# Kernel tuning notes

Hardware: AMD Instinct MI355X
Metric: run time of the kernel (lower is better)

The kernel has to match this reference:

```python
import jax, jax.numpy as jnp
import numpy as np

N, T, DIN, E, D, L, G = 50000, 1, 7, 800000, 64, 3, 64


def _lin(key, fi, fo):
    k1, k2 = jax.random.split(key)
    s = 1.0 / np.sqrt(fi)
    return (jax.random.uniform(k1, (fi, fo), jnp.float32, -s, s),
            jax.random.uniform(k2, (fo,), jnp.float32, -s, s))


def setup_inputs() -> dict:
    key = jax.random.key(0)
    ks = jax.random.split(key, 16)
    x = jax.random.normal(ks[0], (N, T, DIN), jnp.float32)
    edge_index = jax.random.randint(ks[1], (2, E), 0, N).astype(jnp.int64)
    edge_attr = jax.random.uniform(ks[2], (E, T), jnp.float32)
    batch = jnp.sort(jax.random.randint(ks[3], (N,), 0, G)).astype(jnp.int64)
    degree = jax.random.uniform(ks[4], (N,), jnp.float32)
    W_en, b_en = _lin(ks[5], DIN, D)
    W_ene, b_ene = _lin(ks[6], DIN + 1, D - 1)
    W_agg, b_agg = _lin(ks[7], D, D)
    Wm = []; bm = []; Wu = []; bu = []
    for l in range(L):
        w, b = _lin(jax.random.fold_in(ks[8], l), 2 * D, D); Wm.append(w); bm.append(b)
        w, b = _lin(jax.random.fold_in(ks[9], l), 2 * D, D); Wu.append(w); bu.append(b)
    Wm = jnp.stack(Wm); bm = jnp.stack(bm); Wu = jnp.stack(Wu); bu = jnp.stack(bu)
    W_g, b_g = _lin(ks[10], D, D)
    W_r, b_r = _lin(ks[11], 2 * D, 1)
    return dict(x=x, edge_index=edge_index, edge_attr=edge_attr, batch=batch,
                degree=degree, num_graphs=G,
                W_en=W_en, b_en=b_en, W_ene=W_ene, b_ene=b_ene,
                W_agg=W_agg, b_agg=b_agg, Wm=Wm, bm=bm, Wu=Wu, bu=bu,
                W_g=W_g, b_g=b_g, W_r=W_r, b_r=b_r)


def _scatter_mean(vals, idx, n):
    # vals: [M, T, F] -> [n, T, F]; empty segments -> 0 (count clamped to 1)
    s = jax.ops.segment_sum(vals, idx, num_segments=n)
    c = jax.ops.segment_sum(jnp.ones((vals.shape[0], 1, 1), vals.dtype), idx, num_segments=n)
    return s / jnp.maximum(c, 1.0)


def reference(x, edge_index, edge_attr, batch, degree, num_graphs,
              W_en, b_en, W_ene, b_ene, W_agg, b_agg,
              Wm, bm, Wu, bu, W_g, b_g, W_r, b_r):
    relu = jax.nn.relu
    col, row = edge_index[0], edge_index[1]
    n = x.shape[0]
    x_emb = relu(x @ W_en + b_en)                                   # [N,T,D]
    # node+edge embedding: gather source nodes, append edge_attr, mean over dst
    ne_in = jnp.concatenate([x[col], edge_attr[:, :, None]], axis=-1)  # [E,T,DIN+1]
    node_edge = _scatter_mean(ne_in, row, n)                        # [N,T,DIN+1]
    node_edge = relu(node_edge @ W_ene + b_ene)                     # [N,T,D-1]
    deg_max = jax.ops.segment_max(degree, batch, num_segments=num_graphs)
    degree_norm = deg_max[batch][:, None, None]                     # [N,1,1] -> broadcast over T
    degree_norm = jnp.broadcast_to(degree_norm, (n, node_edge.shape[1], 1))
    x_agg_emb = relu(jnp.concatenate([node_edge, degree_norm], axis=-1) @ W_agg + b_agg)
    for l in range(Wm.shape[0]):
        x_agg = _scatter_mean(edge_attr[:, :, None] * x_emb[col], row, n)   # [N,T,D]
        m = relu(jnp.concatenate([x_agg, x_agg_emb], axis=-1) @ Wm[l] + bm[l])
        x_emb = relu(jnp.concatenate([x_emb, m], axis=-1) @ Wu[l] + bu[l])
    g_agg = _scatter_mean(x_emb, batch, num_graphs)                 # [G,T,D]
    g_agg = g_agg @ W_g + b_g
    inp = jnp.concatenate([g_agg[batch], x_emb], axis=-1)           # [N,T,2D]
    q = relu(inp) @ W_r + b_r                                       # [N,T,1]
    return jnp.squeeze(q, axis=-1)                                  # [N,T]
```

## Files before the change

kernel.cpp:

```cpp
#include <hip/hip_runtime.h>

constexpr int NN  = 50000;
constexpr int EE  = 800000;
constexpr int GG  = 64;
constexpr int LL  = 3;

__device__ __forceinline__ float reluf(float x) { return x > 0.f ? x : 0.f; }

__global__ void k_count(const int* __restrict__ ei, int* __restrict__ cnt,
                        int* __restrict__ rel) {
    int e = blockIdx.x * blockDim.x + threadIdx.x;
    if (e >= EE) return;
    rel[e] = atomicAdd(&cnt[ei[EE + e]], 1);
}

__global__ void k_scan1(const int* __restrict__ cnt, int* __restrict__ off,
                        int* __restrict__ bsum,
                        const int* __restrict__ batch, const float* __restrict__ degree,
                        unsigned* __restrict__ degmax_u) {
    __shared__ int s[256];
    __shared__ unsigned smax[GG];
    int t = threadIdx.x, blk = blockIdx.x;
    if (t < GG) smax[t] = 0u;
    int base = blk * 1024 + t * 4;
    int v[4], tot = 0;
#pragma unroll
    for (int j = 0; j < 4; j++) {
        int i = base + j;
        v[j] = (i < NN) ? cnt[i] : 0;
        tot += v[j];
    }
    s[t] = tot;
    __syncthreads();
    {
        int curb = -1; unsigned cur = 0u;
#pragma unroll
        for (int j = 0; j < 4; j++) {
            int i = base + j;
            if (i < NN) {
                int b = batch[i];
                unsigned d = __float_as_uint(degree[i]);
                if (b != curb) {
                    if (curb >= 0) atomicMax(&smax[curb], cur);
                    curb = b; cur = d;
                } else if (d > cur) cur = d;
            }
        }
        if (curb >= 0) atomicMax(&smax[curb], cur);
    }
    for (int d = 1; d < 256; d <<= 1) {
        int a = (t >= d) ? s[t - d] : 0;
        __syncthreads();
        s[t] += a;
        __syncthreads();
    }
    int run = s[t] - tot;
#pragma unroll
    for (int j = 0; j < 4; j++) {
        int i = base + j;
        if (i <= NN) off[i] = run;
        run += v[j];
    }
    if (t == 255) bsum[blk] = s[255];
    __syncthreads();
    if (t < GG && smax[t] != 0u) atomicMax(&degmax_u[t], smax[t]);
}
__global__ void k_scan2(int* __restrict__ bsum, int nb) {
    if (threadIdx.x == 0) {
        int run = 0;
        for (int b = 0; b < nb; b++) { int t = bsum[b]; bsum[b] = run; run += t; }
    }
}
__global__ void k_scan3(int* __restrict__ off, const int* __restrict__ bsum) {
    int i = blockIdx.x * blockDim.x + threadIdx.x;
    if (i <= NN) off[i] += bsum[i >> 10];
}

__global__ void k_fill(const int* __restrict__ ei, const float* __restrict__ ea,
                       const int* __restrict__ off, const int* __restrict__ rel,
                       int2* __restrict__ sorted) {
    int e = blockIdx.x * blockDim.x + threadIdx.x;
    if (e >= EE) return;
    int col = ei[e];
    int row = ei[EE + e];
    sorted[off[row] + rel[e]] = make_int2(col, __float_as_int(ea[e]));
}

__global__ void k_nesum(const float* __restrict__ x, const int2* __restrict__ sorted,
                        const int* __restrict__ off, float* __restrict__ ne_sum) {
    int gwave = (blockIdx.x * blockDim.x + threadIdx.x) >> 6;
    int lane = threadIdx.x & 63;
    int sub = lane >> 3;
    int f = lane & 7;
    int node = gwave * 8 + sub;
    if (node >= NN) return;
    int jb = off[node], je = off[node + 1];
    float a0 = 0.f, a1 = 0.f, a2 = 0.f, a3 = 0.f;
    int j = jb;
    for (; j + 4 <= je; j += 4) {
        int2 p0 = sorted[j], p1 = sorted[j + 1], p2 = sorted[j + 2], p3 = sorted[j + 3];
        a0 += (f < 7) ? x[(size_t)p0.x * 7 + f] : __int_as_float(p0.y);
        a1 += (f < 7) ? x[(size_t)p1.x * 7 + f] : __int_as_float(p1.y);
        a2 += (f < 7) ? x[(size_t)p2.x * 7 + f] : __int_as_float(p2.y);
        a3 += (f < 7) ? x[(size_t)p3.x * 7 + f] : __int_as_float(p3.y);
    }
    for (; j < je; j++) {
        int2 p = sorted[j];
        a0 += (f < 7) ? x[(size_t)p.x * 7 + f] : __int_as_float(p.y);
    }
    ne_sum[(size_t)node * 8 + f] = (a0 + a1) + (a2 + a3);
}

__global__ __launch_bounds__(256) void k_node_pre(
        const float* __restrict__ x, const int* __restrict__ cnt,
        const float* __restrict__ ne_sum, const unsigned* __restrict__ degmax_u,
        const int* __restrict__ batch,
        const float* __restrict__ W_en, const float* __restrict__ b_en,
        const float* __restrict__ W_ene, const float* __restrict__ b_ene,
        float* __restrict__ x_emb, float* __restrict__ agg_in) {
    __shared__ float sWen[7 * 64], sben[64];
    __shared__ float sWene[8 * 63], sbene[63];
    for (int i = threadIdx.x; i < 7 * 64; i += 256) sWen[i] = W_en[i];
    for (int i = threadIdx.x; i < 64; i += 256) sben[i] = b_en[i];
    for (int i = threadIdx.x; i < 8 * 63; i += 256) sWene[i] = W_ene[i];
    for (int i = threadIdx.x; i < 63; i += 256) sbene[i] = b_ene[i];
    __syncthreads();
    int lane = threadIdx.x & 63;
    int slot = threadIdx.x >> 6;
    int wave = blockIdx.x * 4 + slot;
    int nw = gridDim.x * 4;
    for (int i = wave; i < NN; i += nw) {
        float acc = sben[lane];
#pragma unroll
        for (int k = 0; k < 7; k++) acc += x[(size_t)i * 7 + k] * sWen[k * 64 + lane];
        x_emb[(size_t)i * 64 + lane] = reluf(acc);
        float c = (float)cnt[i]; if (c < 1.f) c = 1.f;
        float rc = 1.f / c;
        int oo = lane < 63 ? lane : 0;
        float na = sbene[oo];
#pragma unroll
        for (int k = 0; k < 8; k++) na += (ne_sum[(size_t)i * 8 + k] * rc) * sWene[k * 63 + oo];
        na = reluf(na);
        float dn = __uint_as_float(degmax_u[batch[i]]);
        agg_in[(size_t)i * 64 + lane] = (lane < 63) ? na : dn;
    }
}

template <int MODE>
__global__ __launch_bounds__(256) void k_mv64(
        const float* __restrict__ in, const float* __restrict__ W,
        const float* __restrict__ b, const float* __restrict__ tmp,
        float* __restrict__ out, int nwaves) {
    __shared__ float sbuf[4][2][64];
    int slot = threadIdx.x >> 6;
    int gwave = (blockIdx.x * blockDim.x + threadIdx.x) >> 6;
    int lane = threadIdx.x & 63;
    int per = (NN + nwaves - 1) / nwaves;
    int n0 = gwave * per;
    int n1 = n0 + per; if (n1 > NN) n1 = NN;
    if (n0 >= n1) return;
    float w[64];
#pragma unroll
    for (int k = 0; k < 64; k++) w[k] = W[(size_t)k * 64 + lane];
    float bias = (MODE == 0) ? 0.f : b[lane];
    sbuf[slot][0][lane] = in[(size_t)n0 * 64 + lane];
    int cntn = n1 - n0;
    for (int i = 0; i < cntn; i++) {
        int n = n0 + i;
        size_t oA = (size_t)n * 64 + lane;
        float tv = (MODE == 1) ? tmp[oA] : 0.f;
        float vnext = 0.f;
        if (i + 1 < cntn) vnext = in[(size_t)(n + 1) * 64 + lane];
        const float* bufp = &sbuf[slot][i & 1][0];
        float a0 = 0.f, a1 = 0.f;
#pragma unroll
        for (int kb = 0; kb < 64; kb += 8) {
            float4 x0 = *(const float4*)(bufp + kb);
            float4 x1 = *(const float4*)(bufp + kb + 4);
            a0 = fmaf(x0.x, w[kb + 0], a0); a1 = fmaf(x0.y, w[kb + 1], a1);
            a0 = fmaf(x0.z, w[kb + 2], a0); a1 = fmaf(x0.w, w[kb + 3], a1);
            a0 = fmaf(x1.x, w[kb + 4], a0); a1 = fmaf(x1.y, w[kb + 5], a1);
            a0 = fmaf(x1.z, w[kb + 6], a0); a1 = fmaf(x1.w, w[kb + 7], a1);
        }
        float r = a0 + a1;
        if (MODE == 0)      out[oA] = r;
        else if (MODE == 1) out[oA] = reluf(r + tv + bias);
        else                out[oA] = reluf(r + bias);
        if (i + 1 < cntn) sbuf[slot][(i + 1) & 1][lane] = vnext;
    }
}

__global__ __launch_bounds__(256) void k_layer_agg(
        const float* __restrict__ xemb, const int* __restrict__ off,
        const int* __restrict__ cnt, const int2* __restrict__ sorted,
        float* __restrict__ xagg) {
    int lane = threadIdx.x & 63;
    int slot = threadIdx.x >> 6;
    int wave = blockIdx.x * 4 + slot;
    int nw = gridDim.x * 4;
    for (int i = wave; i < NN; i += nw) {
        int jb = off[i], je = off[i + 1];
        float a0 = 0.f, a1 = 0.f, a2 = 0.f, a3 = 0.f;
        float a4 = 0.f, a5 = 0.f, a6 = 0.f, a7 = 0.f;
        int j = jb;
        for (; j + 8 <= je; j += 8) {
            int2 p0 = sorted[j + 0], p1 = sorted[j + 1];
            int2 p2 = sorted[j + 2], p3 = sorted[j + 3];
            int2 p4 = sorted[j + 4], p5 = sorted[j + 5];
            int2 p6 = sorted[j + 6], p7 = sorted[j + 7];
            a0 = fmaf(__int_as_float(p0.y), xemb[(size_t)p0.x * 64 + lane], a0);
            a1 = fmaf(__int_as_float(p1.y), xemb[(size_t)p1.x * 64 + lane], a1);
            a2 = fmaf(__int_as_float(p2.y), xemb[(size_t)p2.x * 64 + lane], a2);
            a3 = fmaf(__int_as_float(p3.y), xemb[(size_t)p3.x * 64 + lane], a3);
            a4 = fmaf(__int_as_float(p4.y), xemb[(size_t)p4.x * 64 + lane], a4);
            a5 = fmaf(__int_as_float(p5.y), xemb[(size_t)p5.x * 64 + lane], a5);
            a6 = fmaf(__int_as_float(p6.y), xemb[(size_t)p6.x * 64 + lane], a6);
            a7 = fmaf(__int_as_float(p7.y), xemb[(size_t)p7.x * 64 + lane], a7);
        }
        if (j < je) {
            int jl = je - 1;
            int2 p0 = sorted[j + 0];
            int2 p1 = sorted[min(j + 1, jl)];
            int2 p2 = sorted[min(j + 2, jl)];
            int2 p3 = sorted[min(j + 3, jl)];
            int2 p4 = sorted[min(j + 4, jl)];
            int2 p5 = sorted[min(j + 5, jl)];
            int2 p6 = sorted[min(j + 6, jl)];
            int2 p7 = sorted[min(j + 7, jl)];
            float s0 = __int_as_float(p0.y);
            float s1 = (j + 1 < je) ? __int_as_float(p1.y) : 0.f;
            float s2 = (j + 2 < je) ? __int_as_float(p2.y) : 0.f;
            float s3 = (j + 3 < je) ? __int_as_float(p3.y) : 0.f;
            float s4 = (j + 4 < je) ? __int_as_float(p4.y) : 0.f;
            float s5 = (j + 5 < je) ? __int_as_float(p5.y) : 0.f;
            float s6 = (j + 6 < je) ? __int_as_float(p6.y) : 0.f;
            float s7 = (j + 7 < je) ? __int_as_float(p7.y) : 0.f;
            a0 = fmaf(s0, xemb[(size_t)p0.x * 64 + lane], a0);
            a1 = fmaf(s1, xemb[(size_t)p1.x * 64 + lane], a1);
            a2 = fmaf(s2, xemb[(size_t)p2.x * 64 + lane], a2);
            a3 = fmaf(s3, xemb[(size_t)p3.x * 64 + lane], a3);
            a4 = fmaf(s4, xemb[(size_t)p4.x * 64 + lane], a4);
            a5 = fmaf(s5, xemb[(size_t)p5.x * 64 + lane], a5);
            a6 = fmaf(s6, xemb[(size_t)p6.x * 64 + lane], a6);
            a7 = fmaf(s7, xemb[(size_t)p7.x * 64 + lane], a7);
        }
        float acc = ((a0 + a1) + (a2 + a3)) + ((a4 + a5) + (a6 + a7));
        float c = (float)cnt[i]; if (c < 1.f) c = 1.f;
        xagg[(size_t)i * 64 + lane] = acc * (1.f / c);
    }
}

constexpr int CHUNK = 32;
__global__ void k_graph_sum(const float* __restrict__ xemb, const int* __restrict__ batch,
                            float* __restrict__ g_sum, int* __restrict__ g_cnt) {
    int wave = (blockIdx.x * blockDim.x + threadIdx.x) >> 6;
    int lane = threadIdx.x & 63;
    int i0 = wave * CHUNK;
    if (i0 >= NN) return;
    int i1 = i0 + CHUNK; if (i1 > NN) i1 = NN;
    int curb = batch[i0];
    float acc = 0.f;
    int ncnt = 0;
    for (int i = i0; i < i1; i++) {
        int b = batch[i];
        if (b != curb) {
            unsafeAtomicAdd(&g_sum[curb * 64 + lane], acc);
            if (lane == 0) atomicAdd(&g_cnt[curb], ncnt);
            acc = 0.f; ncnt = 0; curb = b;
        }
        acc += xemb[(size_t)i * 64 + lane];
        ncnt++;
    }
    unsafeAtomicAdd(&g_sum[curb * 64 + lane], acc);
    if (lane == 0) atomicAdd(&g_cnt[curb], ncnt);
}

__global__ void k_graph_emb(const float* __restrict__ g_sum, const int* __restrict__ g_cnt,
                            const float* __restrict__ W_g, const float* __restrict__ b_g,
                            float* __restrict__ g_agg) {
    __shared__ float sin[4 * 64];
    int lane = threadIdx.x & 63;
    int slot = threadIdx.x >> 6;
    int g = blockIdx.x * 4 + slot;
    if (g >= GG) return;
    float c = (float)g_cnt[g]; if (c < 1.f) c = 1.f;
    sin[slot * 64 + lane] = g_sum[g * 64 + lane] * (1.f / c);
    __syncthreads();
    float acc = b_g[lane];
    for (int k = 0; k < 64; k++) acc += sin[slot * 64 + k] * W_g[k * 64 + lane];
    g_agg[g * 64 + lane] = acc;
}

__global__ void k_readout(const float* __restrict__ g_agg, const float* __restrict__ xemb,
                          const int* __restrict__ batch,
                          const float* __restrict__ W_r, const float* __restrict__ b_r,
                          float* __restrict__ out) {
    int i = blockIdx.x * blockDim.x + threadIdx.x;
    if (i >= NN) return;
    int b = batch[i];
    float acc = b_r[0];
    const float* ga = g_agg + (size_t)b * 64;
    const float* xe = xemb + (size_t)i * 64;
#pragma unroll 8
    for (int k = 0; k < 64; k++) acc += reluf(ga[k]) * W_r[k];
#pragma unroll 8
    for (int k = 0; k < 64; k++) acc += reluf(xe[k]) * W_r[64 + k];
    out[i] = acc;
}

extern "C" void kernel_launch(void* const* d_in, const int* in_sizes, int n_in,
                              void* d_out, int out_size, void* d_ws, size_t ws_size,
                              hipStream_t stream) {
    const float* x      = (const float*)d_in[0];
    const int*   ei     = (const int*)d_in[1];
    const float* ea     = (const float*)d_in[2];
    const int*   batch  = (const int*)d_in[3];
    const float* degree = (const float*)d_in[4];
    const float* W_en  = (const float*)d_in[6];
    const float* b_en  = (const float*)d_in[7];
    const float* W_ene = (const float*)d_in[8];
    const float* b_ene = (const float*)d_in[9];
    const float* W_agg = (const float*)d_in[10];
    const float* b_agg = (const float*)d_in[11];
    const float* Wm    = (const float*)d_in[12];
    const float* bm    = (const float*)d_in[13];
    const float* Wu    = (const float*)d_in[14];
    const float* bu    = (const float*)d_in[15];
    const float* W_g   = (const float*)d_in[16];
    const float* b_g   = (const float*)d_in[17];
    const float* W_r   = (const float*)d_in[18];
    const float* b_r   = (const float*)d_in[19];
    float* out = (float*)d_out;

    char* ws = (char*)d_ws;
    size_t o = 0;
    int*      cnt      = (int*)(ws + o * 4);      o += NN;
    unsigned* degmax_u = (unsigned*)(ws + o * 4); o += GG;
    float*    g_sum    = (float*)(ws + o * 4);    o += GG * 64;
    int*      g_cnt    = (int*)(ws + o * 4);      o += GG;
    size_t zero_bytes = o * 4;
    int*      off      = (int*)(ws + o * 4);      o += NN + 1;
    int*      bsum     = (int*)(ws + o * 4);      o += 64;
    int*      rel      = (int*)(ws + o * 4);      o += EE;
    float*    ne_sum   = (float*)(ws + o * 4);    o += (size_t)NN * 8;
    o = (o + 1) & ~(size_t)1;
    int2*     sorted   = (int2*)(ws + o * 4);     o += (size_t)EE * 2;
    float*    agg_in   = (float*)(ws + o * 4);    o += (size_t)NN * 64;
    float*    xae      = (float*)(ws + o * 4);    o += (size_t)NN * 64;
    float*    xA       = (float*)(ws + o * 4);    o += (size_t)NN * 64;
    float*    xB       = (float*)(ws + o * 4);    o += (size_t)NN * 64;
    float*    xagg     = (float*)(ws + o * 4);    o += (size_t)NN * 64;
    float*    mbuf     = (float*)(ws + o * 4);    o += (size_t)NN * 64;
    float*    tmpb     = (float*)(ws + o * 4);    o += (size_t)NN * 64;
    float*    g_agg    = (float*)(ws + o * 4);    o += GG * 64;

    hipMemsetAsync(d_ws, 0, zero_bytes, stream);

    const int NB_SCAN = 49;
    const int MV_BLOCKS = 1024;
    const int MV_WAVES = MV_BLOCKS * 4;
    k_count<<<(EE + 255) / 256, 256, 0, stream>>>(ei, cnt, rel);
    k_scan1<<<NB_SCAN, 256, 0, stream>>>(cnt, off, bsum, batch, degree, degmax_u);
    k_scan2<<<1, 64, 0, stream>>>(bsum, NB_SCAN);
    k_scan3<<<(NN + 256) / 256, 256, 0, stream>>>(off, bsum);
    k_fill<<<(EE + 255) / 256, 256, 0, stream>>>(ei, ea, off, rel, sorted);
    k_nesum<<<((NN + 7) / 8 * 64 + 255) / 256, 256, 0, stream>>>(x, sorted, off, ne_sum);
    k_node_pre<<<512, 256, 0, stream>>>(x, cnt, ne_sum, degmax_u, batch,
                                        W_en, b_en, W_ene, b_ene, xA, agg_in);
    k_mv64<2><<<MV_BLOCKS, 256, 0, stream>>>(agg_in, W_agg, b_agg, nullptr, xae, MV_WAVES);
    const float* cur = xA;
    float* nxt = xB;
    for (int l = 0; l < LL; l++) {
        const float* WmL = Wm + (size_t)l * 128 * 64;
        const float* WuL = Wu + (size_t)l * 128 * 64;
        k_layer_agg<<<2048, 256, 0, stream>>>(cur, off, cnt, sorted, xagg);
        k_mv64<0><<<MV_BLOCKS, 256, 0, stream>>>(xagg, WmL, nullptr, nullptr, tmpb, MV_WAVES);
        k_mv64<1><<<MV_BLOCKS, 256, 0, stream>>>(xae, WmL + 64 * 64, bm + l * 64, tmpb,
                                                 mbuf, MV_WAVES);
        k_mv64<0><<<MV_BLOCKS, 256, 0, stream>>>(cur, WuL, nullptr, nullptr, tmpb, MV_WAVES);
        k_mv64<1><<<MV_BLOCKS, 256, 0, stream>>>(mbuf, WuL + 64 * 64, bu + l * 64, tmpb,
                                                 nxt, MV_WAVES);
        float* t = (float*)cur; cur = nxt; nxt = t;
    }
    int gs_waves = (NN + CHUNK - 1) / CHUNK;
    k_graph_sum<<<(gs_waves * 64 + 255) / 256, 256, 0, stream>>>(cur, batch, g_sum, g_cnt);
    k_graph_emb<<<16, 256, 0, stream>>>(g_sum, g_cnt, W_g, b_g, g_agg);
    k_readout<<<(NN + 255) / 256, 256, 0, stream>>>(g_agg, cur, batch, W_r, b_r, out);
}
```

Baseline: 489.3 us.

## Fuse split 64-wide matvecs into 128-wide kernels and fold graph sum into last layer

Replaces the pairs of 64-input matvec kernels (which passed partial sums through a temp buffer) with a single 128-input kernel that reads both concatenated halves, removing the tmp buffer round trip and halving launches per layer. The W_agg matvec is folded into k_node_pre using wave shuffles, the graph node count moves into the scan kernel, and the graph sum is accumulated inside the final update kernel, removing k_graph_sum. The 128-register weight array raises register pressure, with launch bounds and block count adjusted to compensate.

After: 483.2 us. About the same (-1.2%).

```diff
diff --git a/kernel.cpp b/kernel.cpp
--- a/kernel.cpp
+++ b/kernel.cpp
@@ -17,11 +17,12 @@
 __global__ void k_scan1(const int* __restrict__ cnt, int* __restrict__ off,
                         int* __restrict__ bsum,
                         const int* __restrict__ batch, const float* __restrict__ degree,
-                        unsigned* __restrict__ degmax_u) {
+                        unsigned* __restrict__ degmax_u, int* __restrict__ g_cnt) {
     __shared__ int s[256];
     __shared__ unsigned smax[GG];
+    __shared__ int scnt[GG];
     int t = threadIdx.x, blk = blockIdx.x;
-    if (t < GG) smax[t] = 0u;
+    if (t < GG) { smax[t] = 0u; scnt[t] = 0; }
     int base = blk * 1024 + t * 4;
     int v[4], tot = 0;
 #pragma unroll
@@ -33,7 +34,7 @@
     s[t] = tot;
     __syncthreads();
     {
-        int curb = -1; unsigned cur = 0u;
+        int curb = -1; unsigned cur = 0u; int ccnt = 0;
 #pragma unroll
         for (int j = 0; j < 4; j++) {
             int i = base + j;
@@ -41,12 +42,15 @@
                 int b = batch[i];
                 unsigned d = __float_as_uint(degree[i]);
                 if (b != curb) {
-                    if (curb >= 0) atomicMax(&smax[curb], cur);
-                    curb = b; cur = d;
-                } else if (d > cur) cur = d;
+                    if (curb >= 0) { atomicMax(&smax[curb], cur); atomicAdd(&scnt[curb], ccnt); }
+                    curb = b; cur = d; ccnt = 1;
+                } else {
+                    if (d > cur) cur = d;
+                    ccnt++;
+                }
             }
         }
-        if (curb >= 0) atomicMax(&smax[curb], cur);
+        if (curb >= 0) { atomicMax(&smax[curb], cur); atomicAdd(&scnt[curb], ccnt); }
     }
     for (int d = 1; d < 256; d <<= 1) {
         int a = (t >= d) ? s[t - d] : 0;
@@ -63,7 +67,10 @@
     }
     if (t == 255) bsum[blk] = s[255];
     __syncthreads();
-    if (t < GG && smax[t] != 0u) atomicMax(&degmax_u[t], smax[t]);
+    if (t < GG) {
+        if (smax[t] != 0u) atomicMax(&degmax_u[t], smax[t]);
+        if (scnt[t] != 0)  atomicAdd(&g_cnt[t], scnt[t]);
+    }
 }
 __global__ void k_scan2(int* __restrict__ bsum, int nb) {
     if (threadIdx.x == 0) {
@@ -117,7 +124,8 @@
         const int* __restrict__ batch,
         const float* __restrict__ W_en, const float* __restrict__ b_en,
         const float* __restrict__ W_ene, const float* __restrict__ b_ene,
-        float* __restrict__ x_emb, float* __restrict__ agg_in) {
+        const float* __restrict__ W_agg, const float* __restrict__ b_agg,
+        float* __restrict__ x_emb, float* __restrict__ xae) {
     __shared__ float sWen[7 * 64], sben[64];
     __shared__ float sWene[8 * 63], sbene[63];
     for (int i = threadIdx.x; i < 7 * 64; i += 256) sWen[i] = W_en[i];
@@ -129,6 +137,10 @@
     int slot = threadIdx.x >> 6;
     int wave = blockIdx.x * 4 + slot;
     int nw = gridDim.x * 4;
+    float wagg[64];
+#pragma unroll
+    for (int k = 0; k < 64; k++) wagg[k] = W_agg[(size_t)k * 64 + lane];
+    float bagg = b_agg[lane];
     for (int i = wave; i < NN; i += nw) {
         float acc = sben[lane];
 #pragma unroll
@@ -142,16 +154,21 @@
         for (int k = 0; k < 8; k++) na += (ne_sum[(size_t)i * 8 + k] * rc) * sWene[k * 63 + oo];
         na = reluf(na);
         float dn = __uint_as_float(degmax_u[batch[i]]);
-        agg_in[(size_t)i * 64 + lane] = (lane < 63) ? na : dn;
-    }
-}
-
-template <int MODE>
-__global__ __launch_bounds__(256) void k_mv64(
-        const float* __restrict__ in, const float* __restrict__ W,
-        const float* __restrict__ b, const float* __restrict__ tmp,
-        float* __restrict__ out, int nwaves) {
-    __shared__ float sbuf[4][2][64];
+        float val = (lane < 63) ? na : dn;
+        float acc2 = bagg;
+#pragma unroll
+        for (int k = 0; k < 64; k++) acc2 = fmaf(__shfl(val, k, 64), wagg[k], acc2);
+        xae[(size_t)i * 64 + lane] = reluf(acc2);
+    }
+}
+
+template <int GSUM>
+__global__ __launch_bounds__(256, 3) void k_mv128(
+        const float* __restrict__ inA, const float* __restrict__ inB,
+        const float* __restrict__ W, const float* __restrict__ b,
+        float* __restrict__ out, int nwaves,
+        const int* __restrict__ batch, float* __restrict__ g_sum) {
+    __shared__ float sbuf[4][2][128];
     int slot = threadIdx.x >> 6;
     int gwave = (blockIdx.x * blockDim.x + threadIdx.x) >> 6;
     int lane = threadIdx.x & 63;
@@ -159,22 +176,26 @@
     int n0 = gwave * per;
     int n1 = n0 + per; if (n1 > NN) n1 = NN;
     if (n0 >= n1) return;
-    float w[64];
-#pragma unroll
-    for (int k = 0; k < 64; k++) w[k] = W[(size_t)k * 64 + lane];
-    float bias = (MODE == 0) ? 0.f : b[lane];
-    sbuf[slot][0][lane] = in[(size_t)n0 * 64 + lane];
+    float w[128];
+#pragma unroll
+    for (int k = 0; k < 128; k++) w[k] = W[(size_t)k * 64 + lane];
+    float bias = b[lane];
+    sbuf[slot][0][lane]      = inA[(size_t)n0 * 64 + lane];
+    sbuf[slot][0][64 + lane] = inB[(size_t)n0 * 64 + lane];
     int cntn = n1 - n0;
+    float gacc = 0.f;
+    int curb = GSUM ? batch[n0] : 0;
     for (int i = 0; i < cntn; i++) {
         int n = n0 + i;
-        size_t oA = (size_t)n * 64 + lane;
-        float tv = (MODE == 1) ? tmp[oA] : 0.f;
-        float vnext = 0.f;
-        if (i + 1 < cntn) vnext = in[(size_t)(n + 1) * 64 + lane];
+        float vA = 0.f, vB = 0.f;
+        if (i + 1 < cntn) {
+            vA = inA[(size_t)(n + 1) * 64 + lane];
+            vB = inB[(size_t)(n + 1) * 64 + lane];
+        }
         const float* bufp = &sbuf[slot][i & 1][0];
         float a0 = 0.f, a1 = 0.f;
 #pragma unroll
-        for (int kb = 0; kb < 64; kb += 8) {
+        for (int kb = 0; kb < 128; kb += 8) {
             float4 x0 = *(const float4*)(bufp + kb);
             float4 x1 = *(const float4*)(bufp + kb + 4);
             a0 = fmaf(x0.x, w[kb + 0], a0); a1 = fmaf(x0.y, w[kb + 1], a1);
@@ -182,12 +203,22 @@
             a0 = fmaf(x1.x, w[kb + 4], a0); a1 = fmaf(x1.y, w[kb + 5], a1);
             a0 = fmaf(x1.z, w[kb + 6], a0); a1 = fmaf(x1.w, w[kb + 7], a1);
         }
-        float r = a0 + a1;
-        if (MODE == 0)      out[oA] = r;
-        else if (MODE == 1) out[oA] = reluf(r + tv + bias);
-        else                out[oA] = reluf(r + bias);
-        if (i + 1 < cntn) sbuf[slot][(i + 1) & 1][lane] = vnext;
-    }
+        float r = reluf(a0 + a1 + bias);
+        out[(size_t)n * 64 + lane] = r;
+        if (GSUM) {
+            int bb = batch[n];
+            if (bb != curb) {
+                unsafeAtomicAdd(&g_sum[curb * 64 + lane], gacc);
+                gacc = 0.f; curb = bb;
+            }
+            gacc += r;
+        }
+        if (i + 1 < cntn) {
+            sbuf[slot][(i + 1) & 1][lane]      = vA;
+            sbuf[slot][(i + 1) & 1][64 + lane] = vB;
+        }
+    }
+    if (GSUM) unsafeAtomicAdd(&g_sum[curb * 64 + lane], gacc);
 }
 
 __global__ __launch_bounds__(256) void k_layer_agg(
@@ -250,31 +281,6 @@
     }
 }
 
-constexpr int CHUNK = 32;
-__global__ void k_graph_sum(const float* __restrict__ xemb, const int* __restrict__ batch,
-                            float* __restrict__ g_sum, int* __restrict__ g_cnt) {
-    int wave = (blockIdx.x * blockDim.x + threadIdx.x) >> 6;
-    int lane = threadIdx.x & 63;
-    int i0 = wave * CHUNK;
-    if (i0 >= NN) return;
-    int i1 = i0 + CHUNK; if (i1 > NN) i1 = NN;
-    int curb = batch[i0];
-    float acc = 0.f;
-    int ncnt = 0;
-    for (int i = i0; i < i1; i++) {
-        int b = batch[i];
-        if (b != curb) {
-            unsafeAtomicAdd(&g_sum[curb * 64 + lane], acc);
-            if (lane == 0) atomicAdd(&g_cnt[curb], ncnt);
-            acc = 0.f; ncnt = 0; curb = b;
-        }
-        acc += xemb[(size_t)i * 64 + lane];
-        ncnt++;
-    }
-    unsafeAtomicAdd(&g_sum[curb * 64 + lane], acc);
-    if (lane == 0) atomicAdd(&g_cnt[curb], ncnt);
-}
-
 __global__ void k_graph_emb(const float* __restrict__ g_sum, const int* __restrict__ g_cnt,
                             const float* __restrict__ W_g, const float* __restrict__ b_g,
                             float* __restrict__ g_agg) {
@@ -345,45 +351,44 @@
     float*    ne_sum   = (float*)(ws + o * 4);    o += (size_t)NN * 8;
     o = (o + 1) & ~(size_t)1;
     int2*     sorted   = (int2*)(ws + o * 4);     o += (size_t)EE * 2;
-    float*    agg_in   = (float*)(ws + o * 4);    o += (size_t)NN * 64;
     float*    xae      = (float*)(ws + o * 4);    o += (size_t)NN * 64;
     float*    xA       = (float*)(ws + o * 4);    o += (size_t)NN * 64;
     float*    xB       = (float*)(ws + o * 4);    o += (size_t)NN * 64;
     float*    xagg     = (float*)(ws + o * 4);    o += (size_t)NN * 64;
     float*    mbuf     = (float*)(ws + o * 4);    o += (size_t)NN * 64;
-    float*    tmpb     = (float*)(ws + o * 4);    o += (size_t)NN * 64;
     float*    g_agg    = (float*)(ws + o * 4);    o += GG * 64;
 
     hipMemsetAsync(d_ws, 0, zero_bytes, stream);
 
     const int NB_SCAN = 49;
-    const int MV_BLOCKS = 1024;
+    const int MV_BLOCKS = 768;
     const int MV_WAVES = MV_BLOCKS * 4;
     k_count<<<(EE + 255) / 256, 256, 0, stream>>>(ei, cnt, rel);
-    k_scan1<<<NB_SCAN, 256, 0, stream>>>(cnt, off, bsum, batch, degree, degmax_u);
+    k_scan1<<<NB_SCAN, 256, 0, stream>>>(cnt, off, bsum, batch, degree, degmax_u, g_cnt);
     k_scan2<<<1, 64, 0, stream>>>(bsum, NB_SCAN);
     k_scan3<<<(NN + 256) / 256, 256, 0, stream>>>(off, bsum);
     k_fill<<<(EE + 255) / 256, 256, 0, stream>>>(ei, ea, off, rel, sorted);
     k_nesum<<<((NN + 7) / 8 * 64 + 255) / 256, 256, 0, stream>>>(x, sorted, off, ne_sum);
     k_node_pre<<<512, 256, 0, stream>>>(x, cnt, ne_sum, degmax_u, batch,
-                                        W_en, b_en, W_ene, b_ene, xA, agg_in);
-    k_mv64<2><<<MV_BLOCKS, 256, 0, stream>>>(agg_in, W_agg, b_agg, nullptr, xae, MV_WAVES);
+                                        W_en, b_en, W_ene, b_ene, W_agg, b_agg,
+                                        xA, xae);
     const float* cur = xA;
     float* nxt = xB;
     for (int l = 0; l < LL; l++) {
         const float* WmL = Wm + (size_t)l * 128 * 64;
         const float* WuL = Wu + (size_t)l * 128 * 64;
         k_layer_agg<<<2048, 256, 0, stream>>>(cur, off, cnt, sorted, xagg);
-        k_mv64<0><<<MV_BLOCKS, 256, 0, stream>>>(xagg, WmL, nullptr, nullptr, tmpb, MV_WAVES);
-        k_mv64<1><<<MV_BLOCKS, 256, 0, stream>>>(xae, WmL + 64 * 64, bm + l * 64, tmpb,
-                                                 mbuf, MV_WAVES);
-        k_mv64<0><<<MV_BLOCKS, 256, 0, stream>>>(cur, WuL, nullptr, nullptr, tmpb, MV_WAVES);
-        k_mv64<1><<<MV_BLOCKS, 256, 0, stream>>>(mbuf, WuL + 64 * 64, bu + l * 64, tmpb,
-                                                 nxt, MV_WAVES);
+        k_mv128<0><<<MV_BLOCKS, 256, 0, stream>>>(xagg, xae, WmL, bm + l * 64,
+                                                  mbuf, MV_WAVES, nullptr, nullptr);
+        if (l < LL - 1) {
+            k_mv128<0><<<MV_BLOCKS, 256, 0, stream>>>(cur, mbuf, WuL, bu + l * 64,
+                                                      nxt, MV_WAVES, nullptr, nullptr);
+        } else {
+            k_mv128<1><<<MV_BLOCKS, 256, 0, stream>>>(cur, mbuf, WuL, bu + l * 64,
+                                                      nxt, MV_WAVES, batch, g_sum);
+        }
         float* t = (float*)cur; cur = nxt; nxt = t;
     }
-    int gs_waves = (NN + CHUNK - 1) / CHUNK;
-    k_graph_sum<<<(gs_waves * 64 + 255) / 256, 256, 0, stream>>>(cur, batch, g_sum, g_cnt);
     k_graph_emb<<<16, 256, 0, stream>>>(g_sum, g_cnt, W_g, b_g, g_agg);
     k_readout<<<(NN + 255) / 256, 256, 0, stream>>>(g_agg, cur, batch, W_r, b_r, out);
 }
```
